# Performance work log

Hardware: AMD Instinct MI355X
Metric: run time of the kernel (lower is better)

## Reference

```python
import jax, jax.numpy as jnp
import numpy as np

N = 100000
E = 1600000
IN_FEATS = 512
N_CLASSES = 40
H1, D1 = 8, 8
H2, D2 = 1, N_CLASSES


def gat_conv(x, src, dst, W, al, ar, b, H, D):
    # x: [N, F] -> h: [N, H, D]
    n = x.shape[0]
    h = (x @ W).reshape(n, H, D)
    el = (h * al[None]).sum(-1)  # [N, H]
    er = (h * ar[None]).sum(-1)  # [N, H]
    e = jax.nn.leaky_relu(el[src] + er[dst], 0.2)  # [E, H]
    # segment softmax over destination neighborhoods
    emax = jax.ops.segment_max(e, dst, num_segments=n)  # [N, H]
    ee = jnp.exp(e - emax[dst])
    denom = jax.ops.segment_sum(ee, dst, num_segments=n)  # [N, H]
    a = ee / (denom[dst] + 1e-9)  # [E, H]
    m = h[src] * a[:, :, None]  # [E, H, D]
    out = jax.ops.segment_sum(m, dst, num_segments=n)  # [N, H, D]
    return out + b.reshape(1, H, D)


def setup_inputs() -> dict:
    key = jax.random.key(0)
    ks = jax.random.split(key, 12)
    g1 = 1.0 / np.sqrt(IN_FEATS)
    g2 = 1.0 / np.sqrt(H1 * D1)
    return {
        "x": jax.random.normal(ks[0], (N, IN_FEATS), jnp.float32),
        "src": jax.random.randint(ks[1], (E,), 0, N, jnp.int32),
        "dst": jax.random.randint(ks[2], (E,), 0, N, jnp.int32),
        "W1": jax.random.normal(ks[3], (IN_FEATS, H1 * D1), jnp.float32) * g1,
        "al1": jax.random.normal(ks[4], (H1, D1), jnp.float32) * 0.1,
        "ar1": jax.random.normal(ks[5], (H1, D1), jnp.float32) * 0.1,
        "b1": jnp.zeros((H1 * D1,), jnp.float32),
        "W2": jax.random.normal(ks[6], (H1 * D1, H2 * D2), jnp.float32) * g2,
        "al2": jax.random.normal(ks[7], (H2, D2), jnp.float32) * 0.1,
        "ar2": jax.random.normal(ks[8], (H2, D2), jnp.float32) * 0.1,
        "b2": jnp.zeros((H2 * D2,), jnp.float32),
    }


def reference(x, src, dst, W1, al1, ar1, b1, W2, al2, ar2, b2):
    h = gat_conv(x, src, dst, W1, al1, ar1, b1, H1, D1)  # [N, 8, 8]
    h = jax.nn.elu(h.reshape(N, H1 * D1))  # [N, 64]
    h = gat_conv(h, src, dst, W2, al2, ar2, b2, H2, D2).mean(axis=1)  # [N, n_classes]
    return jax.nn.log_softmax(h, axis=1)
```

## Files before the change

### kernel.cpp

```cpp
#include <hip/hip_runtime.h>
#include <hip/hip_bf16.h>
#include <math.h>

#define NCLS 40
#define PWG 256
#define BSH 9
#define NBMAX 512
#define SRCB 23
#define CSRCAP 14336

typedef __attribute__((ext_vector_type(8))) short bf16x8;
typedef __attribute__((ext_vector_type(4))) float f32x4;

__device__ inline float bf2f(ushort u) {
    unsigned v = ((unsigned)u) << 16;
    float f;
    __builtin_memcpy(&f, &v, 4);
    return f;
}
__device__ inline ushort f2bf(float f) {
    unsigned v;
    __builtin_memcpy(&v, &f, 4);
    unsigned r = (v + 0x7FFFu + ((v >> 16) & 1u)) >> 16;
    return (ushort)r;
}

__global__ __launch_bounds__(256) void conv_prep_kernel(
    const float* __restrict__ W1, ushort* __restrict__ W1t,
    const float* __restrict__ W2, const float* __restrict__ al2,
    const float* __restrict__ ar2, float* __restrict__ wal2,
    float* __restrict__ war2)
{
    if (blockIdx.x < 128) {
        int id = blockIdx.x * 256 + threadIdx.x;
        int k = id >> 6, c = id & 63;
        W1t[c * 512 + k] = f2bf(W1[k * 64 + c]);
    } else {
        int k = threadIdx.x;
        if (k < 64) {
            float a = 0.f, b = 0.f;
            for (int c = 0; c < NCLS; c++) {
                float w = W2[k * NCLS + c];
                a += w * al2[c];
                b += w * ar2[c];
            }
            wal2[k] = a;
            war2[k] = b;
        }
    }
}

__global__ __launch_bounds__(256) void gemm1_mfma_kernel(
    const float* __restrict__ x, const ushort* __restrict__ W1t,
    ushort* __restrict__ h1b, int Nn)
{
    __shared__ ushort As[64 * 40];
    __shared__ ushort Bs[64 * 40];
    const int t = threadIdx.x;
    const int lane = t & 63, w = t >> 6;
    const int tile = blockIdx.x * 64;

    f32x4 acc[4] = {};

    const int sr = t >> 2;
    const int sk = (t & 3) * 8;
    const int arow = tile + sr;
    const bool rowok = arow < Nn;
    const float* xrow = x + (size_t)arow * 512;
    const ushort* wrow = W1t + (size_t)sr * 512;

    const int r = lane & 15, g = lane >> 4;

    float4 f0, f1;
    bf16x8 bv;
    if (rowok) {
        f0 = *(const float4*)(xrow + sk);
        f1 = *(const float4*)(xrow + sk + 4);
    } else {
        f0 = make_float4(0.f, 0.f, 0.f, 0.f);
        f1 = f0;
    }
    bv = *(const bf16x8*)(wrow + sk);

    for (int k0 = 0; k0 < 512; k0 += 32) {
        bf16x8 av;
        av[0] = (short)f2bf(f0.x); av[1] = (short)f2bf(f0.y);
        av[2] = (short)f2bf(f0.z); av[3] = (short)f2bf(f0.w);
        av[4] = (short)f2bf(f1.x); av[5] = (short)f2bf(f1.y);
        av[6] = (short)f2bf(f1.z); av[7] = (short)f2bf(f1.w);
        *(bf16x8*)&As[sr * 40 + sk] = av;
        *(bf16x8*)&Bs[sr * 40 + sk] = bv;
        __syncthreads();

        int k1 = k0 + 32;
        if (k1 < 512) {
            if (rowok) {
                f0 = *(const float4*)(xrow + k1 + sk);
                f1 = *(const float4*)(xrow + k1 + sk + 4);
            }
            bv = *(const bf16x8*)(wrow + k1 + sk);
        }

        bf16x8 afrag = *(const bf16x8*)&As[(w * 16 + r) * 40 + g * 8];
#pragma unroll
        for (int cb = 0; cb < 4; cb++) {
            bf16x8 bfrag = *(const bf16x8*)&Bs[(cb * 16 + r) * 40 + g * 8];
            acc[cb] = __builtin_amdgcn_mfma_f32_16x16x32_bf16(afrag, bfrag, acc[cb], 0, 0, 0);
        }
        __syncthreads();
    }

#pragma unroll
    for (int cb = 0; cb < 4; cb++) {
#pragma unroll
        for (int v = 0; v < 4; v++) {
            int row = tile + w * 16 + g * 4 + v;
            if (row < Nn) h1b[(size_t)row * 64 + cb * 16 + r] = f2bf(acc[cb][v]);
        }
    }
}

__global__ __launch_bounds__(256) void elr1_kernel(
    const ushort* __restrict__ h1b, const float* __restrict__ al1,
    const float* __restrict__ ar1, float* __restrict__ el1,
    float* __restrict__ er1, int Nn)
{
    int id = blockIdx.x * 256 + threadIdx.x;
    if (id >= Nn * 8) return;
    int h = id & 7;
    const ushort* p = h1b + (size_t)id * 8;
    ushort4 u0 = *(const ushort4*)p;
    ushort4 u1 = *(const ushort4*)(p + 4);
    float v0 = bf2f(u0.x), v1 = bf2f(u0.y), v2 = bf2f(u0.z), v3 = bf2f(u0.w);
    float v4 = bf2f(u1.x), v5 = bf2f(u1.y), v6 = bf2f(u1.z), v7 = bf2f(u1.w);
    const float* a = al1 + h * 8;
    const float* b = ar1 + h * 8;
    el1[id] = v0 * a[0] + v1 * a[1] + v2 * a[2] + v3 * a[3] + v4 * a[4] + v5 * a[5] + v6 * a[6] + v7 * a[7];
    er1[id] = v0 * b[0] + v1 * b[1] + v2 * b[2] + v3 * b[3] + v4 * b[4] + v5 * b[5] + v6 * b[6] + v7 * b[7];
}

__global__ __launch_bounds__(256) void hist_kernel(const int* __restrict__ dst,
                                                   int* __restrict__ hist,
                                                   int Ee, int chunk, int NB)
{
    __shared__ int lh[NBMAX];
    const int wg = blockIdx.x, tid = threadIdx.x;
    for (int i = tid; i < NB; i += 256) lh[i] = 0;
    __syncthreads();
    const int beg = wg * chunk;
    const int endv = min(Ee, beg + chunk);
    for (int i = beg + tid; i < endv; i += 256) atomicAdd(&lh[dst[i] >> BSH], 1);
    __syncthreads();
    for (int b = tid; b < NB; b += 256) hist[b * PWG + wg] = lh[b];
}

__global__ __launch_bounds__(256) void scanA_kernel(int* __restrict__ hist,
                                                    int* __restrict__ bucketTot)
{
    __shared__ int s[256];
    const int b = blockIdx.x, tid = threadIdx.x;
    int v = hist[b * PWG + tid];
    s[tid] = v;
    __syncthreads();
#pragma unroll
    for (int o = 1; o < 256; o <<= 1) {
        int t = (tid >= o) ? s[tid - o] : 0;
        __syncthreads();
        s[tid] += t;
        __syncthreads();
    }
    hist[b * PWG + tid] = s[tid] - v;
    if (tid == 255) bucketTot[b] = s[255];
}

__global__ __launch_bounds__(256) void scanB_kernel(const int* __restrict__ bucketTot,
                                                    int* __restrict__ bucketBase,
                                                    int NB, int Ee)
{
    __shared__ int s[256];
    const int tid = threadIdx.x;
    int v = (tid < NB) ? bucketTot[tid] : 0;
    s[tid] = v;
    __syncthreads();
#pragma unroll
    for (int o = 1; o < 256; o <<= 1) {
        int t = (tid >= o) ? s[tid - o] : 0;
        __syncthreads();
        s[tid] += t;
        __syncthreads();
    }
    if (tid < NB) bucketBase[tid] = s[tid] - v;
    if (tid == 0) bucketBase[NB] = Ee;
}

__global__ __launch_bounds__(256) void partition_kernel(const int* __restrict__ src,
                                                        const int* __restrict__ dst,
                                                        const int* __restrict__ hist,
                                                        const int* __restrict__ bucketBase,
                                                        unsigned* __restrict__ ebuf,
                                                        int Ee, int chunk, int NB)
{
    __shared__ int cur[NBMAX];
    const int wg = blockIdx.x, tid = threadIdx.x;
    for (int b = tid; b < NB; b += 256) cur[b] = hist[b * PWG + wg] + bucketBase[b];
    __syncthreads();
    const int beg = wg * chunk;
    const int endv = min(Ee, beg + chunk);
    for (int i = beg + tid; i < endv; i += 256) {
        int d = dst[i];
        int p = atomicAdd(&cur[d >> BSH], 1);
        ebuf[p] = ((unsigned)(d & ((1 << BSH) - 1)) << SRCB) | (unsigned)src[i];
    }
}

__global__ __launch_bounds__(512) void bucket_csr_kernel(const unsigned* __restrict__ ebuf,
                                                         const int* __restrict__ bucketBase,
                                                         int* __restrict__ row_start,
                                                         int* __restrict__ perm_src,
                                                         int Nn, int Ee, int NB)
{
    __shared__ unsigned stage[CSRCAP];
    __shared__ int cnt[512];
    __shared__ int s[512];
    __shared__ int cur[512];
    const int b = blockIdx.x, tid = threadIdx.x;
    const int base = b << BSH;
    const int bb = bucketBase[b], be = bucketBase[b + 1];
    const int m = be - bb;

    cnt[tid] = 0;
    __syncthreads();
    for (int idx = tid; idx < m; idx += 512) {
        unsigned pk = ebuf[bb + idx];
        if (idx < CSRCAP) stage[idx] = pk;
        atomicAdd(&cnt[pk >> SRCB], 1);
    }
    __syncthreads();
    int v = cnt[tid];
    s[tid] = v;
    __syncthreads();
#pragma unroll
    for (int o = 1; o < 512; o <<= 1) {
        int t = (tid >= o) ? s[tid - o] : 0;
        __syncthreads();
        s[tid] += t;
        __syncthreads();
    }
    const int off = bb + s[tid] - v;
    const int node = base + tid;
    if (node < Nn) row_start[node] = off;
    cur[tid] = off;
    __syncthreads();
    for (int idx = tid; idx < m; idx += 512) {
        unsigned pk = (idx < CSRCAP) ? stage[idx] : ebuf[bb + idx];
        int p = atomicAdd(&cur[pk >> SRCB], 1);
        perm_src[p] = (int)(pk & ((1u << SRCB) - 1u));
    }
    if (b == NB - 1 && tid == 0) row_start[Nn] = Ee;
}

__global__ __launch_bounds__(256) void agg1_kernel(
    const ushort* __restrict__ h1b, const float* __restrict__ el1,
    const float* __restrict__ er1, const int* __restrict__ row_start,
    const int* __restrict__ perm_src, const float* __restrict__ b1,
    ushort* __restrict__ hmidb, int Nn)
{
    int wid = (blockIdx.x * blockDim.x + threadIdx.x) >> 6;
    int lane = threadIdx.x & 63;
    if (wid >= Nn) return;
    const int h = lane >> 3;
    const int beg = row_start[wid], end = row_start[wid + 1];
    const float er = er1[wid * 8 + h];

    float acc = 0.f, denom = 0.f;
    for (int i0 = beg; i0 < end; i0 += 64) {
        int cnt = min(end - i0, 64);
        int pv = (i0 + lane < end) ? perm_src[i0 + lane] : 0;
        int j = 0;
        for (; j + 8 <= cnt; j += 8) {
            int ss[8];
#pragma unroll
            for (int u = 0; u < 8; u++) ss[u] = __shfl(pv, j + u);
            float ev[8];
            ushort rv[8];
#pragma unroll
            for (int u = 0; u < 8; u++) ev[u] = el1[ss[u] * 8 + h];
#pragma unroll
            for (int u = 0; u < 8; u++) rv[u] = h1b[(size_t)ss[u] * 64 + lane];
#pragma unroll
            for (int u = 0; u < 8; u++) {
                float e = ev[u] + er;
                e = (e >= 0.f) ? e : 0.2f * e;
                float w = __expf(fminf(e, 80.f));
                denom += w;
                acc += bf2f(rv[u]) * w;
            }
        }
        for (; j + 4 <= cnt; j += 4) {
            int ss[4];
#pragma unroll
            for (int u = 0; u < 4; u++) ss[u] = __shfl(pv, j + u);
            float ev[4];
            ushort rv[4];
#pragma unroll
            for (int u = 0; u < 4; u++) ev[u] = el1[ss[u] * 8 + h];
#pragma unroll
            for (int u = 0; u < 4; u++) rv[u] = h1b[(size_t)ss[u] * 64 + lane];
#pragma unroll
            for (int u = 0; u < 4; u++) {
                float e = ev[u] + er;
                e = (e >= 0.f) ? e : 0.2f * e;
                float w = __expf(fminf(e, 80.f));
                denom += w;
                acc += bf2f(rv[u]) * w;
            }
        }
        for (; j < cnt; j++) {
            int sI = __shfl(pv, j);
            float e = el1[sI * 8 + h] + er;
            e = (e >= 0.f) ? e : 0.2f * e;
            float w = __expf(fminf(e, 80.f));
            denom += w;
            acc += bf2f(h1b[(size_t)sI * 64 + lane]) * w;
        }
    }
    float v = acc / (denom + 1e-9f) + b1[lane];
    v = (v > 0.f) ? v : expm1f(v);
    hmidb[(size_t)wid * 64 + lane] = f2bf(v);
}

__global__ __launch_bounds__(256) void gemm2_kernel(
    const ushort* __restrict__ hmidb, const float* __restrict__ W2,
    const float* __restrict__ wal2, const float* __restrict__ war2,
    ushort* __restrict__ h2b, float* __restrict__ el2, float* __restrict__ er2,
    int Nn)
{
    __shared__ float w2s[64 * NCLS];
    __shared__ float wals[64], wars[64];
    for (int i = threadIdx.x; i < 64 * NCLS; i += blockDim.x) w2s[i] = W2[i];
    if (threadIdx.x < 64) {
        wals[threadIdx.x] = wal2[threadIdx.x];
        wars[threadIdx.x] = war2[threadIdx.x];
    }
    __syncthreads();
    int n = blockIdx.x * blockDim.x + threadIdx.x;
    if (n >= Nn) return;

    float out[NCLS];
#pragma unroll
    for (int c = 0; c < NCLS; c++) out[c] = 0.f;
    float accel = 0.f, accer = 0.f;

#pragma unroll 4
    for (int k4 = 0; k4 < 16; k4++) {
        ushort4 u = *(const ushort4*)&hmidb[(size_t)n * 64 + k4 * 4];
        float h0 = bf2f(u.x), h1 = bf2f(u.y), h2 = bf2f(u.z), h3 = bf2f(u.w);
        accel += h0 * wals[k4 * 4] + h1 * wals[k4 * 4 + 1] + h2 * wals[k4 * 4 + 2] + h3 * wals[k4 * 4 + 3];
        accer += h0 * wars[k4 * 4] + h1 * wars[k4 * 4 + 1] + h2 * wars[k4 * 4 + 2] + h3 * wars[k4 * 4 + 3];
#pragma unroll
        for (int c = 0; c < NCLS; c++) {
            out[c] += h0 * w2s[(k4 * 4 + 0) * NCLS + c] + h1 * w2s[(k4 * 4 + 1) * NCLS + c] +
                      h2 * w2s[(k4 * 4 + 2) * NCLS + c] + h3 * w2s[(k4 * 4 + 3) * NCLS + c];
        }
    }
    el2[n] = accel;
    er2[n] = accer;
#pragma unroll
    for (int c = 0; c < NCLS; c++) h2b[(size_t)n * NCLS + c] = f2bf(out[c]);
}

__global__ __launch_bounds__(256) void agg2_kernel(
    const ushort* __restrict__ h2b, const float* __restrict__ el2,
    const float* __restrict__ er2, const int* __restrict__ row_start,
    const int* __restrict__ perm_src, const float* __restrict__ b2,
    float* __restrict__ out, int Nn)
{
    int wid = (blockIdx.x * blockDim.x + threadIdx.x) >> 6;
    int lane = threadIdx.x & 63;
    if (wid >= Nn) return;
    const int beg = row_start[wid], end = row_start[wid + 1];
    const float er = er2[wid];
    const bool act = lane < NCLS;
    const int cl = act ? lane : 0;

    float acc = 0.f, denom = 0.f;
    for (int i0 = beg; i0 < end; i0 += 64) {
        int cnt = min(end - i0, 64);
        int pv = (i0 + lane < end) ? perm_src[i0 + lane] : 0;
        int j = 0;
        for (; j + 8 <= cnt; j += 8) {
            int ss[8];
#pragma unroll
            for (int u = 0; u < 8; u++) ss[u] = __shfl(pv, j + u);
            float ev[8];
            ushort rv[8];
#pragma unroll
            for (int u = 0; u < 8; u++) ev[u] = el2[ss[u]];
#pragma unroll
            for (int u = 0; u < 8; u++) rv[u] = h2b[(size_t)ss[u] * NCLS + cl];
#pragma unroll
            for (int u = 0; u < 8; u++) {
                float e = ev[u] + er;
                e = (e >= 0.f) ? e : 0.2f * e;
                float w = __expf(fminf(e, 80.f));
                denom += w;
                acc += bf2f(rv[u]) * w;
            }
        }
        for (; j + 4 <= cnt; j += 4) {
            int ss[4];
#pragma unroll
            for (int u = 0; u < 4; u++) ss[u] = __shfl(pv, j + u);
            float ev[4];
            ushort rv[4];
#pragma unroll
            for (int u = 0; u < 4; u++) ev[u] = el2[ss[u]];
#pragma unroll
            for (int u = 0; u < 4; u++) rv[u] = h2b[(size_t)ss[u] * NCLS + cl];
#pragma unroll
            for (int u = 0; u < 4; u++) {
                float e = ev[u] + er;
                e = (e >= 0.f) ? e : 0.2f * e;
                float w = __expf(fminf(e, 80.f));
                denom += w;
                acc += bf2f(rv[u]) * w;
            }
        }
        for (; j < cnt; j++) {
            int sI = __shfl(pv, j);
            float e = el2[sI] + er;
            e = (e >= 0.f) ? e : 0.2f * e;
            float w = __expf(fminf(e, 80.f));
            denom += w;
            acc += bf2f(h2b[(size_t)sI * NCLS + cl]) * w;
        }
    }
    float v = act ? (acc / (denom + 1e-9f) + b2[lane]) : -1e30f;

    float mx = v;
#pragma unroll
    for (int o = 1; o < 64; o <<= 1) mx = fmaxf(mx, __shfl_xor(mx, o));
    float sx = act ? __expf(v - mx) : 0.f;
#pragma unroll
    for (int o = 1; o < 64; o <<= 1) sx += __shfl_xor(sx, o);
    if (act) out[(size_t)wid * NCLS + lane] = v - mx - __logf(sx);
}

extern "C" void kernel_launch(void* const* d_in, const int* in_sizes, int n_in,
                              void* d_out, int out_size, void* d_ws, size_t ws_size,
                              hipStream_t stream)
{
    const float* x   = (const float*)d_in[0];
    const int*   src = (const int*)d_in[1];
    const int*   dst = (const int*)d_in[2];
    const float* W1  = (const float*)d_in[3];
    const float* al1 = (const float*)d_in[4];
    const float* ar1 = (const float*)d_in[5];
    const float* b1  = (const float*)d_in[6];
    const float* W2  = (const float*)d_in[7];
    const float* al2 = (const float*)d_in[8];
    const float* ar2 = (const float*)d_in[9];
    const float* b2  = (const float*)d_in[10];
    float* out = (float*)d_out;

    const int Nn = in_sizes[0] / 512;
    const int Ee = in_sizes[1];
    const int NB = (Nn + (1 << BSH) - 1) >> BSH;
    const int chunk = (Ee + PWG - 1) / PWG;

    char* wsb = (char*)d_ws;
    size_t off = 0;
    auto alloc = [&](size_t bytes) -> void* {
        off = (off + 15) & ~(size_t)15;
        void* p = wsb + off;
        off += bytes;
        return p;
    };
    ushort* h1b   = (ushort*)alloc((size_t)Nn * 64 * 2);
    ushort* hmidb = (ushort*)alloc((size_t)Nn * 64 * 2);
    ushort* h2b   = (ushort*)alloc((size_t)Nn * NCLS * 2);
    ushort* W1t   = (ushort*)alloc(64 * 512 * 2);
    float* el1  = (float*)alloc((size_t)Nn * 8 * 4);
    float* er1  = (float*)alloc((size_t)Nn * 8 * 4);
    float* el2  = (float*)alloc((size_t)Nn * 4);
    float* er2  = (float*)alloc((size_t)Nn * 4);
    float* wal2 = (float*)alloc(64 * 4);
    float* war2 = (float*)alloc(64 * 4);
    int* row_start  = (int*)alloc((size_t)(Nn + 1) * 4);
    int* hist       = (int*)alloc((size_t)NB * PWG * 4);
    int* bucketTot  = (int*)alloc((size_t)NB * 4);
    int* bucketBase = (int*)alloc((size_t)(NB + 1) * 4);
    int* perm_src   = (int*)alloc((size_t)Ee * 4);
    unsigned* ebuf  = (unsigned*)alloc((size_t)Ee * 4);

    hist_kernel<<<PWG, 256, 0, stream>>>(dst, hist, Ee, chunk, NB);
    scanA_kernel<<<NB, 256, 0, stream>>>(hist, bucketTot);
    scanB_kernel<<<1, 256, 0, stream>>>(bucketTot, bucketBase, NB, Ee);
    partition_kernel<<<PWG, 256, 0, stream>>>(src, dst, hist, bucketBase, ebuf, Ee, chunk, NB);
    bucket_csr_kernel<<<NB, 512, 0, stream>>>(ebuf, bucketBase, row_start, perm_src, Nn, Ee, NB);

    conv_prep_kernel<<<129, 256, 0, stream>>>(W1, W1t, W2, al2, ar2, wal2, war2);
    gemm1_mfma_kernel<<<(Nn + 63) / 64, 256, 0, stream>>>(x, W1t, h1b, Nn);
    elr1_kernel<<<(Nn * 8 + 255) / 256, 256, 0, stream>>>(h1b, al1, ar1, el1, er1, Nn);
    agg1_kernel<<<(Nn + 3) / 4, 256, 0, stream>>>(h1b, el1, er1, row_start, perm_src, b1, hmidb, Nn);

    gemm2_kernel<<<(Nn + 255) / 256, 256, 0, stream>>>(hmidb, W2, wal2, war2, h2b, el2, er2, Nn);
    agg2_kernel<<<(Nn + 3) / 4, 256, 0, stream>>>(h2b, el2, er2, row_start, perm_src, b2, out, Nn);
}
```

Baseline: 265.4 us.

## Fuse attention logit computation into GEMM1 epilogue and double K-step

Removes the separate elr1 kernel by computing el1/er1 in the GEMM1 epilogue from fp32 accumulators with cross-lane shuffle reductions over each head's 8 columns. The GEMM K-tile also grows from 32 to 64, halving the barrier count and loop iterations at the cost of larger shared tiles and more registers. el/er are now computed from fp32 accumulators instead of bf16-rounded h1b, which shifts numerics slightly.

```diff
diff --git a/kernel.cpp b/kernel.cpp
--- a/kernel.cpp
+++ b/kernel.cpp
@@ -52,10 +52,12 @@
 
 __global__ __launch_bounds__(256) void gemm1_mfma_kernel(
     const float* __restrict__ x, const ushort* __restrict__ W1t,
-    ushort* __restrict__ h1b, int Nn)
-{
-    __shared__ ushort As[64 * 40];
-    __shared__ ushort Bs[64 * 40];
+    const float* __restrict__ al1, const float* __restrict__ ar1,
+    ushort* __restrict__ h1b, float* __restrict__ el1,
+    float* __restrict__ er1, int Nn)
+{
+    __shared__ ushort As[64 * 72];
+    __shared__ ushort Bs[64 * 72];
     const int t = threadIdx.x;
     const int lane = t & 63, w = t >> 6;
     const int tile = blockIdx.x * 64;
@@ -63,7 +65,7 @@
     f32x4 acc[4] = {};
 
     const int sr = t >> 2;
-    const int sk = (t & 3) * 8;
+    const int sk = (t & 3) * 16;
     const int arow = tile + sr;
     const bool rowok = arow < Nn;
     const float* xrow = x + (size_t)arow * 512;
@@ -71,72 +73,85 @@
 
     const int r = lane & 15, g = lane >> 4;
 
-    float4 f0, f1;
-    bf16x8 bv;
+    float4 f0 = make_float4(0.f, 0.f, 0.f, 0.f), f1 = f0, f2 = f0, f3 = f0;
+    bf16x8 bv0, bv1;
     if (rowok) {
         f0 = *(const float4*)(xrow + sk);
         f1 = *(const float4*)(xrow + sk + 4);
-    } else {
-        f0 = make_float4(0.f, 0.f, 0.f, 0.f);
-        f1 = f0;
-    }
-    bv = *(const bf16x8*)(wrow + sk);
-
-    for (int k0 = 0; k0 < 512; k0 += 32) {
-        bf16x8 av;
-        av[0] = (short)f2bf(f0.x); av[1] = (short)f2bf(f0.y);
-        av[2] = (short)f2bf(f0.z); av[3] = (short)f2bf(f0.w);
-        av[4] = (short)f2bf(f1.x); av[5] = (short)f2bf(f1.y);
-        av[6] = (short)f2bf(f1.z); av[7] = (short)f2bf(f1.w);
-        *(bf16x8*)&As[sr * 40 + sk] = av;
-        *(bf16x8*)&Bs[sr * 40 + sk] = bv;
-        __syncthreads();
-
-        int k1 = k0 + 32;
+        f2 = *(const float4*)(xrow + sk + 8);
+        f3 = *(const float4*)(xrow + sk + 12);
+    }
+    bv0 = *(const bf16x8*)(wrow + sk);
+    bv1 = *(const bf16x8*)(wrow + sk + 8);
+
+    for (int k0 = 0; k0 < 512; k0 += 64) {
+        bf16x8 av0, av1;
+        av0[0] = (short)f2bf(f0.x); av0[1] = (short)f2bf(f0.y);
+        av0[2] = (short)f2bf(f0.z); av0[3] = (short)f2bf(f0.w);
+        av0[4] = (short)f2bf(f1.x); av0[5] = (short)f2bf(f1.y);
+        av0[6] = (short)f2bf(f1.z); av0[7] = (short)f2bf(f1.w);
+        av1[0] = (short)f2bf(f2.x); av1[1] = (short)f2bf(f2.y);
+        av1[2] = (short)f2bf(f2.z); av1[3] = (short)f2bf(f2.w);
+        av1[4] = (short)f2bf(f3.x); av1[5] = (short)f2bf(f3.y);
+        av1[6] = (short)f2bf(f3.z); av1[7] = (short)f2bf(f3.w);
+        *(bf16x8*)&As[sr * 72 + sk] = av0;
+        *(bf16x8*)&As[sr * 72 + sk + 8] = av1;
+        *(bf16x8*)&Bs[sr * 72 + sk] = bv0;
+        *(bf16x8*)&Bs[sr * 72 + sk + 8] = bv1;
+        __syncthreads();
+
+        int k1 = k0 + 64;
         if (k1 < 512) {
             if (rowok) {
                 f0 = *(const float4*)(xrow + k1 + sk);
                 f1 = *(const float4*)(xrow + k1 + sk + 4);
-            }
-            bv = *(const bf16x8*)(wrow + k1 + sk);
-        }
-
-        bf16x8 afrag = *(const bf16x8*)&As[(w * 16 + r) * 40 + g * 8];
+                f2 = *(const float4*)(xrow + k1 + sk + 8);
+                f3 = *(const float4*)(xrow + k1 + sk + 12);
+            }
+            bv0 = *(const bf16x8*)(wrow + k1 + sk);
+            bv1 = *(const bf16x8*)(wrow + k1 + sk + 8);
+        }
+
+        bf16x8 af0 = *(const bf16x8*)&As[(w * 16 + r) * 72 + g * 8];
+        bf16x8 af1 = *(const bf16x8*)&As[(w * 16 + r) * 72 + 32 + g * 8];
 #pragma unroll
         for (int cb = 0; cb < 4; cb++) {
-            bf16x8 bfrag = *(const bf16x8*)&Bs[(cb * 16 + r) * 40 + g * 8];
-            acc[cb] = __builtin_amdgcn_mfma_f32_16x16x32_bf16(afrag, bfrag, acc[cb], 0, 0, 0);
-        }
-        __syncthreads();
-    }
-
+            bf16x8 bf0 = *(const bf16x8*)&Bs[(cb * 16 + r) * 72 + g * 8];
+            acc[cb] = __builtin_amdgcn_mfma_f32_16x16x32_bf16(af0, bf0, acc[cb], 0, 0, 0);
+        }
+#pragma unroll
+        for (int cb = 0; cb < 4; cb++) {
+            bf16x8 bf1 = *(const bf16x8*)&Bs[(cb * 16 + r) * 72 + 32 + g * 8];
+            acc[cb] = __builtin_amdgcn_mfma_f32_16x16x32_bf16(af1, bf1, acc[cb], 0, 0, 0);
+        }
+        __syncthreads();
+    }
+
+    float alv[4], arv[4];
 #pragma unroll
     for (int cb = 0; cb < 4; cb++) {
-#pragma unroll
-        for (int v = 0; v < 4; v++) {
-            int row = tile + w * 16 + g * 4 + v;
-            if (row < Nn) h1b[(size_t)row * 64 + cb * 16 + r] = f2bf(acc[cb][v]);
-        }
-    }
-}
-
-__global__ __launch_bounds__(256) void elr1_kernel(
-    const ushort* __restrict__ h1b, const float* __restrict__ al1,
-    const float* __restrict__ ar1, float* __restrict__ el1,
-    float* __restrict__ er1, int Nn)
-{
-    int id = blockIdx.x * 256 + threadIdx.x;
-    if (id >= Nn * 8) return;
-    int h = id & 7;
-    const ushort* p = h1b + (size_t)id * 8;
-    ushort4 u0 = *(const ushort4*)p;
-    ushort4 u1 = *(const ushort4*)(p + 4);
-    float v0 = bf2f(u0.x), v1 = bf2f(u0.y), v2 = bf2f(u0.z), v3 = bf2f(u0.w);
-    float v4 = bf2f(u1.x), v5 = bf2f(u1.y), v6 = bf2f(u1.z), v7 = bf2f(u1.w);
-    const float* a = al1 + h * 8;
-    const float* b = ar1 + h * 8;
-    el1[id] = v0 * a[0] + v1 * a[1] + v2 * a[2] + v3 * a[3] + v4 * a[4] + v5 * a[5] + v6 * a[6] + v7 * a[7];
-    er1[id] = v0 * b[0] + v1 * b[1] + v2 * b[2] + v3 * b[3] + v4 * b[4] + v5 * b[5] + v6 * b[6] + v7 * b[7];
+        alv[cb] = al1[cb * 16 + r];
+        arv[cb] = ar1[cb * 16 + r];
+    }
+#pragma unroll
+    for (int v = 0; v < 4; v++) {
+        int row = tile + w * 16 + g * 4 + v;
+        bool ok = row < Nn;
+#pragma unroll
+        for (int cb = 0; cb < 4; cb++) {
+            if (ok) h1b[(size_t)row * 64 + cb * 16 + r] = f2bf(acc[cb][v]);
+            float pel = acc[cb][v] * alv[cb];
+            float per = acc[cb][v] * arv[cb];
+            pel += __shfl_xor(pel, 1); per += __shfl_xor(per, 1);
+            pel += __shfl_xor(pel, 2); per += __shfl_xor(per, 2);
+            pel += __shfl_xor(pel, 4); per += __shfl_xor(per, 4);
+            if (ok && (r & 7) == 0) {
+                int head = cb * 2 + (r >> 3);
+                el1[row * 8 + head] = pel;
+                er1[row * 8 + head] = per;
+            }
+        }
+    }
 }
 
 __global__ __launch_bounds__(256) void hist_kernel(const int* __restrict__ dst,
@@ -500,8 +515,7 @@
     bucket_csr_kernel<<<NB, 512, 0, stream>>>(ebuf, bucketBase, row_start, perm_src, Nn, Ee, NB);
 
     conv_prep_kernel<<<129, 256, 0, stream>>>(W1, W1t, W2, al2, ar2, wal2, war2);
-    gemm1_mfma_kernel<<<(Nn + 63) / 64, 256, 0, stream>>>(x, W1t, h1b, Nn);
-    elr1_kernel<<<(Nn * 8 + 255) / 256, 256, 0, stream>>>(h1b, al1, ar1, el1, er1, Nn);
+    gemm1_mfma_kernel<<<(Nn + 63) / 64, 256, 0, stream>>>(x, W1t, al1, ar1, h1b, el1, er1, Nn);
     agg1_kernel<<<(Nn + 3) / 4, 256, 0, stream>>>(h1b, el1, er1, row_start, perm_src, b1, hmidb, Nn);
 
     gemm2_kernel<<<(Nn + 255) / 256, 256, 0, stream>>>(hmidb, W2, wal2, war2, h2b, el2, er2, Nn);
```

Result: no change. 264.4 us (-0.4%).
